# Kernel optimization log

Hardware: AMD Instinct MI355X
Metric: run time of the kernel (lower is better)

The kernel has to match this reference:

```python
import jax, jax.numpy as jnp
import numpy as np

B, T, W, CIN, H, COUT = 256, 512, 64, 2, 256, 2
FIN = W * CIN  # 128


def setup_inputs() -> dict:
    key = jax.random.key(0)
    ks = jax.random.split(key, 9)
    s = lambda *sh: 1.0 / np.sqrt(sh[0])
    x = jax.random.normal(ks[0], (B, T, W, CIN), dtype=jnp.float32)
    W1 = jax.random.normal(ks[1], (FIN, H), dtype=jnp.float32) * s(FIN)
    b1 = jnp.zeros((H,), dtype=jnp.float32)
    Wk = jax.random.normal(ks[2], (H, 3 * H), dtype=jnp.float32) * s(H)
    Wr = jax.random.normal(ks[3], (H, 3 * H), dtype=jnp.float32) * s(H)
    bi = jnp.zeros((3 * H,), dtype=jnp.float32)
    br = jnp.zeros((3 * H,), dtype=jnp.float32)
    W2 = jax.random.normal(ks[4], (2 * H, W * COUT), dtype=jnp.float32) * s(2 * H)
    b2 = jnp.zeros((W * COUT,), dtype=jnp.float32)
    return {"x": x, "W1": W1, "b1": b1, "Wk": Wk, "Wr": Wr, "bi": bi, "br": br, "W2": W2, "b2": b2}


def _gru_relu(xg, Wr, br):
    # xg: (T, B, 3H) precomputed input-side gates (x @ Wk + bi)
    # Keras GRU v2: reset_after=True, recurrent_activation=sigmoid, activation=relu
    Hd = Wr.shape[0]
    h0 = jnp.zeros((xg.shape[1], Hd), dtype=xg.dtype)

    def step(h, xg_t):
        rec = h @ Wr + br                     # (B, 3H)
        xz, xr, xh = jnp.split(xg_t, 3, axis=-1)
        rz, rr, rh = jnp.split(rec, 3, axis=-1)
        z = jax.nn.sigmoid(xz + rz)
        r = jax.nn.sigmoid(xr + rr)
        hh = jax.nn.relu(xh + r * rh)
        h_new = z * h + (1.0 - z) * hh
        return h_new, None

    h_last, _ = jax.lax.scan(step, h0, xg)
    return h_last


def reference(x, W1, b1, Wk, Wr, bi, br, W2, b2):
    b = x.shape[0]
    xf = x.reshape(b, T, FIN)                 # Reshape((T, W*CIN))
    h1 = jax.nn.relu(xf @ W1 + b1)            # Dense(hidden, relu): (B, T, H)
    xg = jnp.transpose(h1 @ Wk + bi, (1, 0, 2))  # (T, B, 3H)
    h_last = _gru_relu(xg, Wr, br)            # (B, H); output == final_state
    feat = jnp.concatenate([h_last, h_last], axis=-1)  # (B, 2H)
    y = feat @ W2 + b2                        # (B, W*COUT)
    return y.reshape(b, W, COUT)
```

## Files before the change

kernel.cpp:

```cpp
#include <hip/hip_runtime.h>

typedef unsigned short u16;
typedef unsigned int u32;
typedef float f32x4 __attribute__((ext_vector_type(4)));
typedef __bf16 bf16x8 __attribute__((ext_vector_type(8)));
typedef u16 u16x4 __attribute__((ext_vector_type(4)));

#define TB 256
#define TT 512
#define TC 128

__device__ __forceinline__ u16 f2b(float f) {
  u32 x = __float_as_uint(f);
  return (u16)((x + 0x7fffu + ((x >> 16) & 1u)) >> 16);
}
__device__ __forceinline__ u32 pk2(float a, float b) {
  return (u32)f2b(a) | ((u32)f2b(b) << 16);
}
__device__ __forceinline__ u32 pkbf(float a, float b) {
  u32 r;
  asm("v_cvt_pk_bf16_f32 %0, %1, %2" : "=v"(r) : "v"(a), "v"(b));
  return r;
}
__device__ __forceinline__ float blo(u32 u) { return __uint_as_float(u << 16); }
__device__ __forceinline__ float bhi(u32 u) { return __uint_as_float(u & 0xffff0000u); }
__device__ __forceinline__ float sigm(float x) {
  return __builtin_amdgcn_rcpf(1.f + __expf(-x));
}

__global__ void cast4_kernel(const float* __restrict__ in, u16* __restrict__ out, int n4) {
  int i = blockIdx.x * blockDim.x + threadIdx.x;
  for (; i < n4; i += gridDim.x * blockDim.x) {
    f32x4 v = ((const f32x4*)in)[i];
    u16x4 o = { f2b(v[0]), f2b(v[1]), f2b(v[2]), f2b(v[3]) };
    ((u16x4*)out)[i] = o;
  }
}

__global__ void tcast_kernel(const float* __restrict__ in, u16* __restrict__ out, int K, int N) {
  int idx = blockIdx.x * blockDim.x + threadIdx.x;
  if (idx < K * N) {
    int k = idx / N, n = idx % N;
    out[n * K + k] = f2b(in[idx]);
  }
}

__global__ void wrperm_kernel(const float* __restrict__ in, u16* __restrict__ out) {
  int idx = blockIdx.x * blockDim.x + threadIdx.x;
  if (idx < 256 * 768) {
    int k = idx / 768, n = idx % 768;
    int gate = n >> 8, c = n & 255;
    int w = c >> 5, cc = c & 31, l15 = cc >> 1, grp = cc & 1;
    int nt = gate * 2 + grp;
    out[((((w * 6 + nt) << 4) + l15) << 8) + k] = f2b(in[idx]);
  }
}

__global__ void biasmod_kernel(const float* __restrict__ bi, const float* __restrict__ br,
                               float* __restrict__ bm) {
  int n = blockIdx.x * blockDim.x + threadIdx.x;
  if (n < 768) bm[n] = bi[n] + (n < 512 ? br[n] : 0.f);
}

template<int KT, int MODE>
__global__ __launch_bounds__(256) void gemm_bf16(const u16* __restrict__ A, const u16* __restrict__ Bt,
                                                 const float* __restrict__ bias, u16* __restrict__ C,
                                                 int t0) {
  constexpr int K = KT * 32;
  __shared__ u16 As[128 * 40];
  __shared__ u16 Bs[128 * 40];
  const int tid = threadIdx.x;
  const int bm = blockIdx.x, bn = blockIdx.y;
  const int lane = tid & 63, wid = tid >> 6;
  const int l15 = lane & 15, l4 = lane >> 4;
  const int qm = (wid >> 1) * 64, qn = (wid & 1) * 64;

  const int c0 = tid, c1 = tid + 256;
  const int ar0 = (MODE == 0) ? (bm * 128 + (c0 >> 2)) : (bm * 512 + t0 + (c0 >> 2));
  const int ar1 = (MODE == 0) ? (bm * 128 + (c1 >> 2)) : (bm * 512 + t0 + (c1 >> 2));
  const size_t ga0 = (size_t)ar0 * K + (c0 & 3) * 8;
  const size_t ga1 = (size_t)ar1 * K + (c1 & 3) * 8;
  const size_t gb0 = (size_t)(bn * 128 + (c0 >> 2)) * K + (c0 & 3) * 8;
  const size_t gb1 = (size_t)(bn * 128 + (c1 >> 2)) * K + (c1 & 3) * 8;
  const int sa0 = (c0 >> 2) * 40 + (c0 & 3) * 8;
  const int sa1 = (c1 >> 2) * 40 + (c1 & 3) * 8;

  uint4 ra0 = *(const uint4*)(A + ga0);
  uint4 ra1 = *(const uint4*)(A + ga1);
  uint4 rb0 = *(const uint4*)(Bt + gb0);
  uint4 rb1 = *(const uint4*)(Bt + gb1);

  f32x4 acc[4][4] = {};

  for (int kt = 0; kt < KT; ++kt) {
    __syncthreads();
    *(uint4*)(As + sa0) = ra0;
    *(uint4*)(As + sa1) = ra1;
    *(uint4*)(Bs + sa0) = rb0;
    *(uint4*)(Bs + sa1) = rb1;
    __syncthreads();
    if (kt + 1 < KT) {
      const int ko = (kt + 1) * 32;
      ra0 = *(const uint4*)(A + ga0 + ko);
      ra1 = *(const uint4*)(A + ga1 + ko);
      rb0 = *(const uint4*)(Bt + gb0 + ko);
      rb1 = *(const uint4*)(Bt + gb1 + ko);
    }
    bf16x8 af[4], bfr[4];
#pragma unroll
    for (int mt = 0; mt < 4; ++mt)
      af[mt] = *(const bf16x8*)(As + (qm + mt * 16 + l15) * 40 + l4 * 8);
#pragma unroll
    for (int nt = 0; nt < 4; ++nt)
      bfr[nt] = *(const bf16x8*)(Bs + (qn + nt * 16 + l15) * 40 + l4 * 8);
#pragma unroll
    for (int mt = 0; mt < 4; ++mt)
#pragma unroll
      for (int nt = 0; nt < 4; ++nt)
        acc[mt][nt] = __builtin_amdgcn_mfma_f32_16x16x32_bf16(af[mt], bfr[nt], acc[mt][nt], 0, 0, 0);
  }

#pragma unroll
  for (int mt = 0; mt < 4; ++mt) {
#pragma unroll
    for (int nt = 0; nt < 4; ++nt) {
      const int n = bn * 128 + qn + nt * 16 + l15;
      const float bv = bias[n];
#pragma unroll
      for (int j = 0; j < 4; ++j) {
        const int rloc = qm + mt * 16 + l4 * 4 + j;
        float v = acc[mt][nt][j] + bv;
        if (MODE == 0) {
          v = fmaxf(v, 0.f);
          C[(size_t)(bm * 128 + rloc) * 256 + n] = f2b(v);
        } else {
          C[((size_t)bm * 128 + rloc) * 768 + n] = f2b(v);
        }
      }
    }
  }
}

__global__ __launch_bounds__(512, 2) void gru_kernel(const u16* __restrict__ xgc,
                                                     const u16* __restrict__ WrP,
                                                     const float* __restrict__ br,
                                                     float* __restrict__ hstate, int t0) {
  __shared__ u16 hb0[16 * 264];
  __shared__ u16 hb1[16 * 264];
  __shared__ u16 xs0[16 * 776];
  __shared__ u16 xs1[16 * 776];
  const int tid = threadIdx.x, g = blockIdx.x;
  const int lane = tid & 63, wid = tid >> 6;
  const int l15 = lane & 15, l4 = lane >> 4;

  bf16x8 bw[8][6];
#pragma unroll
  for (int kk = 0; kk < 8; ++kk)
#pragma unroll
    for (int nt = 0; nt < 6; ++nt)
      bw[kk][nt] = *(const bf16x8*)(WrP + ((((wid * 6 + nt) << 4) + l15) << 8) + kk * 32 + l4 * 8);

  const int cbase = wid * 32 + l15 * 2;
  const float brh0 = br[512 + cbase];
  const float brh1 = br[512 + cbase + 1];

  const int rs = tid >> 5, ksl = (tid & 31) * 8;
  const u16* xg_row = xgc + (size_t)(g * 16 + rs) * TC * 768 + ksl;
  u16* xw0 = xs0 + rs * 776 + ksl;
  u16* xw1 = xs1 + rs * 776 + ksl;

  f32x4 h0v, h1v;
  if (t0 == 0) {
    h0v = {0.f, 0.f, 0.f, 0.f};
    h1v = {0.f, 0.f, 0.f, 0.f};
  } else {
#pragma unroll
    for (int j = 0; j < 4; ++j) {
      float2 ld = *(const float2*)(hstate + ((size_t)g * 16 + l4 * 4 + j) * 256 + cbase);
      h0v[j] = ld.x; h1v[j] = ld.y;
    }
  }
#pragma unroll
  for (int j = 0; j < 4; ++j)
    *(u32*)(hb0 + (l4 * 4 + j) * 264 + cbase) = pkbf(h0v[j], h1v[j]);

  {
    const uint4 s0 = *(const uint4*)(xg_row);
    const uint4 s1 = *(const uint4*)(xg_row + 256);
    const uint4 s2 = *(const uint4*)(xg_row + 512);
    *(uint4*)(xw0) = s0;
    *(uint4*)(xw0 + 256) = s1;
    *(uint4*)(xw0 + 512) = s2;
  }
  __syncthreads();

#define GRU_STEP(SRC, DST, XRD, XWR, TL)                                                    \
  {                                                                                         \
                      \
    const int tn = ((TL) + 1 < TC) ? ((TL) + 1) : (TC - 1);                                 \
    const u16* xq = xg_row + (size_t)tn * 768;                                              \
    const uint4 s0 = *(const uint4*)(xq);                                                   \
    const uint4 s1 = *(const uint4*)(xq + 256);                                             \
    const uint4 s2 = *(const uint4*)(xq + 512);                                             \
                                        \
    f32x4 a0 = {}, a2 = {}, a4 = {};                                                        \
    _Pragma("unroll")                                                                       \
    for (int kk = 0; kk < 8; ++kk) {                                                        \
      const bf16x8 a = *(const bf16x8*)((SRC) + l15 * 264 + kk * 32 + l4 * 8);              \
      a0 = __builtin_amdgcn_mfma_f32_16x16x32_bf16(a, bw[kk][0], a0, 0, 0, 0);              \
      a2 = __builtin_amdgcn_mfma_f32_16x16x32_bf16(a, bw[kk][2], a2, 0, 0, 0);              \
      a4 = __builtin_amdgcn_mfma_f32_16x16x32_bf16(a, bw[kk][4], a4, 0, 0, 0);              \
    }                                                                                       \
                       \
    u32 xz_[4], xr_[4], xh_[4];                                                             \
    _Pragma("unroll")                                                                       \
    for (int j = 0; j < 4; ++j) {                                                           \
      const u16* xr2 = (XRD) + (l4 * 4 + j) * 776 + cbase;                                  \
      xz_[j] = *(const u32*)(xr2);                                                          \
      xr_[j] = *(const u32*)(xr2 + 256);                                                    \
      xh_[j] = *(const u32*)(xr2 + 512);                                                    \
    }                                                                                       \
                                        \
    f32x4 a1 = {}, a3 = {}, a5 = {};                                                        \
    _Pragma("unroll")                                                                       \
    for (int kk = 0; kk < 8; ++kk) {                                                        \
      const bf16x8 a = *(const bf16x8*)((SRC) + l15 * 264 + kk * 32 + l4 * 8);              \
      a1 = __builtin_amdgcn_mfma_f32_16x16x32_bf16(a, bw[kk][1], a1, 0, 0, 0);              \
      a3 = __builtin_amdgcn_mfma_f32_16x16x32_bf16(a, bw[kk][3], a3, 0, 0, 0);              \
      a5 = __builtin_amdgcn_mfma_f32_16x16x32_bf16(a, bw[kk][5], a5, 0, 0, 0);              \
    }                                                                                       \
            \
    *(uint4*)(XWR) = s0;                                                                    \
    *(uint4*)((XWR) + 256) = s1;                                                            \
    *(uint4*)((XWR) + 512) = s2;                                                            \
                            \
    _Pragma("unroll")                                                                       \
    for (int j = 0; j < 4; ++j) {                                                           \
      const float z0 = sigm(blo(xz_[j]) + a0[j]);                                           \
      const float r0 = sigm(blo(xr_[j]) + a2[j]);                                           \
      const float hh0 = fmaxf(fmaf(r0, a4[j] + brh0, blo(xh_[j])), 0.f);                    \
      h0v[j] = fmaf(z0, h0v[j] - hh0, hh0);                                                 \
    }                                                                                       \
                                                           \
    _Pragma("unroll")                                                                       \
    for (int j = 0; j < 4; ++j) {                                                           \
      const float z1 = sigm(bhi(xz_[j]) + a1[j]);                                           \
      const float r1 = sigm(bhi(xr_[j]) + a3[j]);                                           \
      const float hh1 = fmaxf(fmaf(r1, a5[j] + brh1, bhi(xh_[j])), 0.f);                    \
      h1v[j] = fmaf(z1, h1v[j] - hh1, hh1);                                                 \
      *(u32*)((DST) + (l4 * 4 + j) * 264 + cbase) = pkbf(h0v[j], h1v[j]);                   \
    }                                                                                       \
    __syncthreads();                                                                        \
  }

  for (int tl = 0; tl < TC; tl += 2) {
    GRU_STEP(hb0, hb1, xs0, xw1, tl);
    GRU_STEP(hb1, hb0, xs1, xw0, tl + 1);
  }
#undef GRU_STEP

#pragma unroll
  for (int j = 0; j < 4; ++j) {
    float2 st = {h0v[j], h1v[j]};
    *(float2*)(hstate + ((size_t)g * 16 + l4 * 4 + j) * 256 + cbase) = st;
  }
}

__global__ void out_kernel(const float* __restrict__ h, const float* __restrict__ W2,
                           const float* __restrict__ b2, float* __restrict__ y) {
  const int bb = blockIdx.x, j = threadIdx.x;
  const float* hr = h + (size_t)bb * 256;
  float s = b2[j];
  for (int i = 0; i < 256; ++i)
    s = fmaf(hr[i], W2[i * 128 + j] + W2[(i + 256) * 128 + j], s);
  y[(size_t)bb * 128 + j] = s;
}

extern "C" void kernel_launch(void* const* d_in, const int* in_sizes, int n_in,
                              void* d_out, int out_size, void* d_ws, size_t ws_size,
                              hipStream_t stream) {
  const float* x  = (const float*)d_in[0];
  const float* W1 = (const float*)d_in[1];
  const float* b1 = (const float*)d_in[2];
  const float* Wk = (const float*)d_in[3];
  const float* Wr = (const float*)d_in[4];
  const float* bi = (const float*)d_in[5];
  const float* br = (const float*)d_in[6];
  const float* W2 = (const float*)d_in[7];
  const float* b2 = (const float*)d_in[8];
  float* y = (float*)d_out;

  const size_t NEED = 67108864ull + 50331648ull + 65536ull + 393216ull + 393216ull + 262144ull + 4096ull;
  if (ws_size < NEED) return;

  char* ws = (char*)d_ws;
  u16* h1    = (u16*)ws;  ws += 67108864;
  u16* xgc   = (u16*)ws;  ws += 50331648;
  u16* W1T   = (u16*)ws;  ws += 65536;
  u16* WkT   = (u16*)ws;  ws += 393216;
  u16* WrP   = (u16*)ws;  ws += 393216;
  float* hstate = (float*)ws; ws += 262144;
  float* biasM  = (float*)ws;
  u16* xb    = xgc;

  cast4_kernel<<<2048, 256, 0, stream>>>(x, xb, 16777216 / 4);
  tcast_kernel<<<128, 256, 0, stream>>>(W1, W1T, 128, 256);
  tcast_kernel<<<768, 256, 0, stream>>>(Wk, WkT, 256, 768);
  wrperm_kernel<<<768, 256, 0, stream>>>(Wr, WrP);
  biasmod_kernel<<<3, 256, 0, stream>>>(bi, br, biasM);
  gemm_bf16<4, 0><<<dim3(1024, 2), 256, 0, stream>>>(xb, W1T, b1, h1, 0);
  for (int c = 0; c < TT / TC; ++c) {
    gemm_bf16<8, 1><<<dim3(256, 6), 256, 0, stream>>>(h1, WkT, biasM, xgc, c * TC);
    gru_kernel<<<16, 512, 0, stream>>>(xgc, WrP, br, hstate, c * TC);
  }
  out_kernel<<<256, 128, 0, stream>>>(hstate, W2, b2, y);
}
```

Before: 1.041 ms.

## Fuse next-chunk input GEMM into GRU kernel to overlap with recurrence

```diff
diff --git a/kernel.cpp b/kernel.cpp
--- a/kernel.cpp
+++ b/kernel.cpp
@@ -8,14 +8,11 @@
 
 #define TB 256
 #define TT 512
-#define TC 128
+#define TC 64
 
 __device__ __forceinline__ u16 f2b(float f) {
   u32 x = __float_as_uint(f);
   return (u16)((x + 0x7fffu + ((x >> 16) & 1u)) >> 16);
-}
-__device__ __forceinline__ u32 pk2(float a, float b) {
-  return (u32)f2b(a) | ((u32)f2b(b) << 16);
 }
 __device__ __forceinline__ u32 pkbf(float a, float b) {
   u32 r;
@@ -76,14 +73,15 @@
   const int qm = (wid >> 1) * 64, qn = (wid & 1) * 64;
 
   const int c0 = tid, c1 = tid + 256;
-  const int ar0 = (MODE == 0) ? (bm * 128 + (c0 >> 2)) : (bm * 512 + t0 + (c0 >> 2));
-  const int ar1 = (MODE == 0) ? (bm * 128 + (c1 >> 2)) : (bm * 512 + t0 + (c1 >> 2));
+  const int r0 = c0 >> 2, r1 = c1 >> 2;
+  const int ar0 = (MODE == 0) ? (bm * 128 + r0) : ((2 * bm + (r0 >> 6)) * 512 + t0 + (r0 & 63));
+  const int ar1 = (MODE == 0) ? (bm * 128 + r1) : ((2 * bm + (r1 >> 6)) * 512 + t0 + (r1 & 63));
   const size_t ga0 = (size_t)ar0 * K + (c0 & 3) * 8;
   const size_t ga1 = (size_t)ar1 * K + (c1 & 3) * 8;
-  const size_t gb0 = (size_t)(bn * 128 + (c0 >> 2)) * K + (c0 & 3) * 8;
-  const size_t gb1 = (size_t)(bn * 128 + (c1 >> 2)) * K + (c1 & 3) * 8;
-  const int sa0 = (c0 >> 2) * 40 + (c0 & 3) * 8;
-  const int sa1 = (c1 >> 2) * 40 + (c1 & 3) * 8;
+  const size_t gb0 = (size_t)(bn * 128 + r0) * K + (c0 & 3) * 8;
+  const size_t gb1 = (size_t)(bn * 128 + r1) * K + (c1 & 3) * 8;
+  const int sa0 = r0 * 40 + (c0 & 3) * 8;
+  const int sa1 = r1 * 40 + (c1 & 3) * 8;
 
   uint4 ra0 = *(const uint4*)(A + ga0);
   uint4 ra1 = *(const uint4*)(A + ga1);
@@ -141,68 +139,72 @@
   }
 }
 
-__global__ __launch_bounds__(512, 2) void gru_kernel(const u16* __restrict__ xgc,
-                                                     const u16* __restrict__ WrP,
-                                                     const float* __restrict__ br,
-                                                     float* __restrict__ hstate, int t0) {
-  __shared__ u16 hb0[16 * 264];
-  __shared__ u16 hb1[16 * 264];
-  __shared__ u16 xs0[16 * 776];
-  __shared__ u16 xs1[16 * 776];
-  const int tid = threadIdx.x, g = blockIdx.x;
-  const int lane = tid & 63, wid = tid >> 6;
-  const int l15 = lane & 15, l4 = lane >> 4;
-
-  bf16x8 bw[8][6];
-#pragma unroll
-  for (int kk = 0; kk < 8; ++kk)
-#pragma unroll
-    for (int nt = 0; nt < 6; ++nt)
-      bw[kk][nt] = *(const bf16x8*)(WrP + ((((wid * 6 + nt) << 4) + l15) << 8) + kk * 32 + l4 * 8);
-
-  const int cbase = wid * 32 + l15 * 2;
-  const float brh0 = br[512 + cbase];
-  const float brh1 = br[512 + cbase + 1];
-
-  const int rs = tid >> 5, ksl = (tid & 31) * 8;
-  const u16* xg_row = xgc + (size_t)(g * 16 + rs) * TC * 768 + ksl;
-  u16* xw0 = xs0 + rs * 776 + ksl;
-  u16* xw1 = xs1 + rs * 776 + ksl;
-
-  f32x4 h0v, h1v;
-  if (t0 == 0) {
-    h0v = {0.f, 0.f, 0.f, 0.f};
-    h1v = {0.f, 0.f, 0.f, 0.f};
-  } else {
-#pragma unroll
-    for (int j = 0; j < 4; ++j) {
-      float2 ld = *(const float2*)(hstate + ((size_t)g * 16 + l4 * 4 + j) * 256 + cbase);
-      h0v[j] = ld.x; h1v[j] = ld.y;
-    }
-  }
-#pragma unroll
-  for (int j = 0; j < 4; ++j)
-    *(u32*)(hb0 + (l4 * 4 + j) * 264 + cbase) = pkbf(h0v[j], h1v[j]);
-
-  {
-    const uint4 s0 = *(const uint4*)(xg_row);
-    const uint4 s1 = *(const uint4*)(xg_row + 256);
-    const uint4 s2 = *(const uint4*)(xg_row + 512);
-    *(uint4*)(xw0) = s0;
-    *(uint4*)(xw0 + 256) = s1;
-    *(uint4*)(xw0 + 512) = s2;
-  }
-  __syncthreads();
+__global__ __launch_bounds__(512, 2) void fused_kernel(
+    const u16* __restrict__ xrd, u16* __restrict__ xwr,
+    const u16* __restrict__ WrP, const float* __restrict__ br,
+    float* __restrict__ hstate, const u16* __restrict__ h1A,
+    const u16* __restrict__ WkT, const float* __restrict__ biasM,
+    int t0, int do_gemm) {
+  __shared__ alignas(16) char smem_c[66560];
+  const int tid = threadIdx.x;
+
+  if (blockIdx.x < 16) {
+    u16* hb0 = (u16*)smem_c;
+    u16* hb1 = (u16*)(smem_c + 8448);
+    u16* xs0 = (u16*)(smem_c + 16896);
+    u16* xs1 = (u16*)(smem_c + 41728);
+    const int g = blockIdx.x;
+    const int lane = tid & 63, wid = tid >> 6;
+    const int l15 = lane & 15, l4 = lane >> 4;
+
+    bf16x8 bw[8][6];
+#pragma unroll
+    for (int kk = 0; kk < 8; ++kk)
+#pragma unroll
+      for (int nt = 0; nt < 6; ++nt)
+        bw[kk][nt] = *(const bf16x8*)(WrP + ((((wid * 6 + nt) << 4) + l15) << 8) + kk * 32 + l4 * 8);
+
+    const int cbase = wid * 32 + l15 * 2;
+    const float brh0 = br[512 + cbase];
+    const float brh1 = br[512 + cbase + 1];
+
+    const int rs = tid >> 5, ksl = (tid & 31) * 8;
+    const u16* xg_row = xrd + (size_t)(g * 16 + rs) * TC * 768 + ksl;
+    u16* xw0 = xs0 + rs * 776 + ksl;
+    u16* xw1 = xs1 + rs * 776 + ksl;
+
+    f32x4 h0v, h1v;
+    if (t0 == 0) {
+      h0v = {0.f, 0.f, 0.f, 0.f};
+      h1v = {0.f, 0.f, 0.f, 0.f};
+    } else {
+#pragma unroll
+      for (int j = 0; j < 4; ++j) {
+        float2 ld = *(const float2*)(hstate + ((size_t)g * 16 + l4 * 4 + j) * 256 + cbase);
+        h0v[j] = ld.x; h1v[j] = ld.y;
+      }
+    }
+#pragma unroll
+    for (int j = 0; j < 4; ++j)
+      *(u32*)(hb0 + (l4 * 4 + j) * 264 + cbase) = pkbf(h0v[j], h1v[j]);
+
+    {
+      const uint4 s0 = *(const uint4*)(xg_row);
+      const uint4 s1 = *(const uint4*)(xg_row + 256);
+      const uint4 s2 = *(const uint4*)(xg_row + 512);
+      *(uint4*)(xw0) = s0;
+      *(uint4*)(xw0 + 256) = s1;
+      *(uint4*)(xw0 + 512) = s2;
+    }
+    __syncthreads();
 
 #define GRU_STEP(SRC, DST, XRD, XWR, TL)                                                    \
   {                                                                                         \
-                      \
     const int tn = ((TL) + 1 < TC) ? ((TL) + 1) : (TC - 1);                                 \
     const u16* xq = xg_row + (size_t)tn * 768;                                              \
     const uint4 s0 = *(const uint4*)(xq);                                                   \
     const uint4 s1 = *(const uint4*)(xq + 256);                                             \
     const uint4 s2 = *(const uint4*)(xq + 512);                                             \
-                                        \
     f32x4 a0 = {}, a2 = {}, a4 = {};                                                        \
     _Pragma("unroll")                                                                       \
     for (int kk = 0; kk < 8; ++kk) {                                                        \
@@ -211,7 +213,6 @@
       a2 = __builtin_amdgcn_mfma_f32_16x16x32_bf16(a, bw[kk][2], a2, 0, 0, 0);              \
       a4 = __builtin_amdgcn_mfma_f32_16x16x32_bf16(a, bw[kk][4], a4, 0, 0, 0);              \
     }                                                                                       \
-                       \
     u32 xz_[4], xr_[4], xh_[4];                                                             \
     _Pragma("unroll")                                                                       \
     for (int j = 0; j < 4; ++j) {                                                           \
@@ -220,7 +221,6 @@
       xr_[j] = *(const u32*)(xr2 + 256);                                                    \
       xh_[j] = *(const u32*)(xr2 + 512);                                                    \
     }                                                                                       \
-                                        \
     f32x4 a1 = {}, a3 = {}, a5 = {};                                                        \
     _Pragma("unroll")                                                                       \
     for (int kk = 0; kk < 8; ++kk) {                                                        \
@@ -229,11 +229,9 @@
       a3 = __builtin_amdgcn_mfma_f32_16x16x32_bf16(a, bw[kk][3], a3, 0, 0, 0);              \
       a5 = __builtin_amdgcn_mfma_f32_16x16x32_bf16(a, bw[kk][5], a5, 0, 0, 0);              \
     }                                                                                       \
-            \
     *(uint4*)(XWR) = s0;                                                                    \
     *(uint4*)((XWR) + 256) = s1;                                                            \
     *(uint4*)((XWR) + 512) = s2;                                                            \
-                            \
     _Pragma("unroll")                                                                       \
     for (int j = 0; j < 4; ++j) {                                                           \
       const float z0 = sigm(blo(xz_[j]) + a0[j]);                                           \
@@ -241,7 +239,6 @@
       const float hh0 = fmaxf(fmaf(r0, a4[j] + brh0, blo(xh_[j])), 0.f);                    \
       h0v[j] = fmaf(z0, h0v[j] - hh0, hh0);                                                 \
     }                                                                                       \
-                                                           \
     _Pragma("unroll")                                                                       \
     for (int j = 0; j < 4; ++j) {                                                           \
       const float z1 = sigm(bhi(xz_[j]) + a1[j]);                                           \
@@ -253,16 +250,95 @@
     __syncthreads();                                                                        \
   }
 
-  for (int tl = 0; tl < TC; tl += 2) {
-    GRU_STEP(hb0, hb1, xs0, xw1, tl);
-    GRU_STEP(hb1, hb0, xs1, xw0, tl + 1);
-  }
+    for (int tl = 0; tl < TC; tl += 2) {
+      GRU_STEP(hb0, hb1, xs0, xw1, tl);
+      GRU_STEP(hb1, hb0, xs1, xw0, tl + 1);
+    }
 #undef GRU_STEP
 
 #pragma unroll
-  for (int j = 0; j < 4; ++j) {
-    float2 st = {h0v[j], h1v[j]};
-    *(float2*)(hstate + ((size_t)g * 16 + l4 * 4 + j) * 256 + cbase) = st;
+    for (int j = 0; j < 4; ++j) {
+      float2 st = {h0v[j], h1v[j]};
+      *(float2*)(hstate + ((size_t)g * 16 + l4 * 4 + j) * 256 + cbase) = st;
+    }
+  } else {
+    if (!do_gemm) return;
+    u16* As = (u16*)smem_c;
+    u16* Bs = (u16*)(smem_c + 10240);
+    const int bidx = blockIdx.x - 16;
+    const int bm = bidx & 127, bn = bidx >> 7;
+    const int t0g = t0 + TC;
+    const bool act = (tid < 256);
+    const int lane = tid & 63, wid = tid >> 6;
+    const int l15 = lane & 15, l4 = lane >> 4;
+    const int qm = ((wid & 3) >> 1) * 64, qn = (wid & 1) * 64;
+
+    const int c0 = tid & 255, c1 = (tid & 255) + 256;
+    const int r0 = c0 >> 2, r1 = c1 >> 2;
+    const int ar0 = (2 * bm + (r0 >> 6)) * 512 + t0g + (r0 & 63);
+    const int ar1 = (2 * bm + (r1 >> 6)) * 512 + t0g + (r1 & 63);
+    const size_t ga0 = (size_t)ar0 * 256 + (c0 & 3) * 8;
+    const size_t ga1 = (size_t)ar1 * 256 + (c1 & 3) * 8;
+    const size_t gb0 = (size_t)(bn * 128 + r0) * 256 + (c0 & 3) * 8;
+    const size_t gb1 = (size_t)(bn * 128 + r1) * 256 + (c1 & 3) * 8;
+    const int sa0 = r0 * 40 + (c0 & 3) * 8;
+    const int sa1 = r1 * 40 + (c1 & 3) * 8;
+
+    uint4 ra0 = {}, ra1 = {}, rb0 = {}, rb1 = {};
+    if (act) {
+      ra0 = *(const uint4*)(h1A + ga0);
+      ra1 = *(const uint4*)(h1A + ga1);
+      rb0 = *(const uint4*)(WkT + gb0);
+      rb1 = *(const uint4*)(WkT + gb1);
+    }
+    f32x4 acc[4][4] = {};
+
+    for (int kt = 0; kt < 8; ++kt) {
+      __syncthreads();
+      if (act) {
+        *(uint4*)(As + sa0) = ra0;
+        *(uint4*)(As + sa1) = ra1;
+        *(uint4*)(Bs + sa0) = rb0;
+        *(uint4*)(Bs + sa1) = rb1;
+      }
+      __syncthreads();
+      if (act) {
+        if (kt + 1 < 8) {
+          const int ko = (kt + 1) * 32;
+          ra0 = *(const uint4*)(h1A + ga0 + ko);
+          ra1 = *(const uint4*)(h1A + ga1 + ko);
+          rb0 = *(const uint4*)(WkT + gb0 + ko);
+          rb1 = *(const uint4*)(WkT + gb1 + ko);
+        }
+        bf16x8 af[4], bfr[4];
+#pragma unroll
+        for (int mt = 0; mt < 4; ++mt)
+          af[mt] = *(const bf16x8*)(As + (qm + mt * 16 + l15) * 40 + l4 * 8);
+#pragma unroll
+        for (int nt = 0; nt < 4; ++nt)
+          bfr[nt] = *(const bf16x8*)(Bs + (qn + nt * 16 + l15) * 40 + l4 * 8);
+#pragma unroll
+        for (int mt = 0; mt < 4; ++mt)
+#pragma unroll
+          for (int nt = 0; nt < 4; ++nt)
+            acc[mt][nt] = __builtin_amdgcn_mfma_f32_16x16x32_bf16(af[mt], bfr[nt], acc[mt][nt], 0, 0, 0);
+      }
+    }
+
+    if (act) {
+#pragma unroll
+      for (int mt = 0; mt < 4; ++mt)
+#pragma unroll
+        for (int nt = 0; nt < 4; ++nt) {
+          const int n = bn * 128 + qn + nt * 16 + l15;
+          const float bv = biasM[n];
+#pragma unroll
+          for (int j = 0; j < 4; ++j) {
+            const int rloc = qm + mt * 16 + l4 * 4 + j;
+            xwr[((size_t)bm * 128 + rloc) * 768 + n] = f2b(acc[mt][nt][j] + bv);
+          }
+        }
+    }
   }
 }
 
@@ -290,18 +366,20 @@
   const float* b2 = (const float*)d_in[8];
   float* y = (float*)d_out;
 
-  const size_t NEED = 67108864ull + 50331648ull + 65536ull + 393216ull + 393216ull + 262144ull + 4096ull;
+  const size_t NEED = 67108864ull + 25165824ull + 25165824ull + 65536ull + 393216ull +
+                      393216ull + 262144ull + 4096ull;
   if (ws_size < NEED) return;
 
   char* ws = (char*)d_ws;
   u16* h1    = (u16*)ws;  ws += 67108864;
-  u16* xgc   = (u16*)ws;  ws += 50331648;
+  u16* xg0   = (u16*)ws;  ws += 25165824;
+  u16* xg1   = (u16*)ws;  ws += 25165824;
   u16* W1T   = (u16*)ws;  ws += 65536;
   u16* WkT   = (u16*)ws;  ws += 393216;
   u16* WrP   = (u16*)ws;  ws += 393216;
   float* hstate = (float*)ws; ws += 262144;
   float* biasM  = (float*)ws;
-  u16* xb    = xgc;
+  u16* xb    = xg0;
 
   cast4_kernel<<<2048, 256, 0, stream>>>(x, xb, 16777216 / 4);
   tcast_kernel<<<128, 256, 0, stream>>>(W1, W1T, 128, 256);
@@ -309,9 +387,12 @@
   wrperm_kernel<<<768, 256, 0, stream>>>(Wr, WrP);
   biasmod_kernel<<<3, 256, 0, stream>>>(bi, br, biasM);
   gemm_bf16<4, 0><<<dim3(1024, 2), 256, 0, stream>>>(xb, W1T, b1, h1, 0);
+  gemm_bf16<8, 1><<<dim3(128, 6), 256, 0, stream>>>(h1, WkT, biasM, xg0, 0);
   for (int c = 0; c < TT / TC; ++c) {
-    gemm_bf16<8, 1><<<dim3(256, 6), 256, 0, stream>>>(h1, WkT, biasM, xgc, c * TC);
-    gru_kernel<<<16, 512, 0, stream>>>(xgc, WrP, br, hstate, c * TC);
+    const u16* xrd = (c & 1) ? xg1 : xg0;
+    u16* xwr = (c & 1) ? xg0 : xg1;
+    fused_kernel<<<784, 512, 0, stream>>>(xrd, xwr, WrP, br, hstate, h1, WkT, biasM,
+                                          c * TC, (c < TT / TC - 1) ? 1 : 0);
   }
   out_kernel<<<256, 128, 0, stream>>>(hstate, W2, b2, y);
 }
```

New measurement: 1.016 ms. -2.4%, faster.
